# Optimization experiments

Measured on AMD Instinct MI355X. Metric: run time of the kernel, lower is better.

The kernel has to match this reference:

```python
import jax, jax.numpy as jnp
import numpy as np
from jax import lax

# Model dims (match init_kwargs / input_specs)
B, S, D = 4, 2048, 1024
L, H, K = 4, 4, 4
DH = D // H            # 256 head dim
UP = 1344              # ceil(1.3*D/64)*64, gated FFN proj dim
EPS = 1e-5


def _ln(x, w):
    # xlstm LayerNorm: weight only, no bias
    mu = x.mean(-1, keepdims=True)
    var = x.var(-1, keepdims=True)
    return (x - mu) * lax.rsqrt(var + EPS) * w


def _slstm_layer(xn, cw, cb, wi, wf, wz, wo, rk, b, gnw):
    # xn: (B,S,D). Causal depthwise conv1d + swish feeds i/f gates; z/o from xn.
    Bc, Sc, Dc = xn.shape
    xc = lax.conv_general_dilated(
        xn.transpose(0, 2, 1), cw[:, None, :], (1,), [(K - 1, 0)],
        dimension_numbers=("NCH", "OIH", "NCH"), feature_group_count=Dc)
    xc = jax.nn.silu(xc + cb[None, :, None]).transpose(0, 2, 1)
    hx = xc.reshape(Bc, Sc, H, DH)
    hz = xn.reshape(Bc, Sc, H, DH)
    # LinearHeadwiseExpand: block-diagonal per-head linear, no bias
    gi = jnp.einsum("bshd,hod->bsho", hx, wi)
    gf = jnp.einsum("bshd,hod->bsho", hx, wf)
    gz = jnp.einsum("bshd,hod->bsho", hz, wz)
    go = jnp.einsum("bshd,hod->bsho", hz, wo)
    wx = jnp.stack([gi, gf, gz, go], axis=3)  # (B,S,H,4,DH)

    def step(carry, wx_t):
        h, c, n, m = carry  # each (B,H,DH)
        raw = wx_t + jnp.einsum("bhd,hdgo->bhgo", h, rk) + b  # (B,H,4,DH)
        ir, fr, zr, og = raw[:, :, 0], raw[:, :, 1], raw[:, :, 2], raw[:, :, 3]
        lfm = m + jax.nn.log_sigmoid(fr)
        mn = jnp.maximum(ir, lfm)          # stabilizer state
        ig = jnp.exp(ir - mn)
        fg = jnp.exp(lfm - mn)
        cn = fg * c + ig * jnp.tanh(zr)
        nn = fg * n + ig
        hn = jax.nn.sigmoid(og) * cn / nn
        return (hn, cn, nn, mn), hn

    z0 = jnp.zeros((Bc, H, DH), xn.dtype)
    _, ys = lax.scan(step, (z0, z0, z0, z0), jnp.moveaxis(wx, 1, 0))
    y = jnp.moveaxis(ys, 0, 1)  # (B,S,H,DH)
    # MultiHeadLayerNorm / GroupNorm(num_groups=H), weight only
    mu = y.mean(-1, keepdims=True)
    var = y.var(-1, keepdims=True)
    y = (y - mu) * lax.rsqrt(var + EPS) * gnw.reshape(H, DH)
    return y.reshape(Bc, Sc, Dc)


def _ffn(xn, wu, wd):
    u = xn @ wu
    g, v = u[..., :UP], u[..., UP:]
    return (jax.nn.gelu(g, approximate=False) * v) @ wd


def setup_inputs() -> dict:
    key = jax.random.key(0)
    ks = jax.random.split(key, 9)
    sg = DH ** -0.5
    return {
        "x": jax.random.normal(ks[0], (B, S, D), jnp.float32),
        "ln1_w": jnp.ones((L, D), jnp.float32),
        "conv_w": jax.random.normal(ks[1], (L, D, K), jnp.float32) * 0.1,
        "conv_b": jnp.zeros((L, D), jnp.float32),
        "wi": jax.random.normal(ks[2], (L, H, DH, DH), jnp.float32) * sg,
        "wf": jax.random.normal(ks[3], (L, H, DH, DH), jnp.float32) * sg,
        "wz": jax.random.normal(ks[4], (L, H, DH, DH), jnp.float32) * sg,
        "wo": jax.random.normal(ks[5], (L, H, DH, DH), jnp.float32) * sg,
        "rker": jax.random.normal(ks[6], (L, H, DH, 4, DH), jnp.float32) * sg,
        "cell_b": jax.random.normal(ks[7], (L, H, 4, DH), jnp.float32) * 0.1,
        "gn_w": jnp.ones((L, D), jnp.float32),
        "ln2_w": jnp.ones((L, D), jnp.float32),
        "ff_up": jax.random.normal(ks[8], (L, D, 2 * UP), jnp.float32) * (D ** -0.5),
        "ff_down": jax.random.normal(jax.random.fold_in(key, 99), (L, UP, D), jnp.float32) * (UP ** -0.5),
        "post_w": jnp.ones((D,), jnp.float32),
    }


def reference(x, ln1_w, conv_w, conv_b, wi, wf, wz, wo, rker, cell_b, gn_w, ln2_w, ff_up, ff_down, post_w):
    for l in range(L):
        x = x + _slstm_layer(_ln(x, ln1_w[l]), conv_w[l], conv_b[l],
                             wi[l], wf[l], wz[l], wo[l], rker[l], cell_b[l], gn_w[l])
        x = x + _ffn(_ln(x, ln2_w[l]), ff_up[l], ff_down[l])
    return _ln(x, post_w)  # post-blocks norm; dropout is identity in eval
```

## Files before the change

kernel.cpp:

```cpp
#include <hip/hip_runtime.h>
#include <hip/hip_bf16.h>
#include <hip/hip_fp16.h>
#include <math.h>


typedef unsigned int  u32;
typedef unsigned short u16;
typedef __hip_bfloat16 bf16;

typedef short bf16x8 __attribute__((ext_vector_type(8)));
typedef float f32x4  __attribute__((ext_vector_type(4)));
typedef _Float16 half2t __attribute__((ext_vector_type(2)));

#define EPSF 1e-5f
#define SIGF32 0x3F800000u

__device__ __forceinline__ float bfu2f(u16 u){ return __uint_as_float(((u32)u) << 16); }
__device__ __forceinline__ float ldm(const void* p, long i, int f32){
  return f32 ? ((const float*)p)[i] : bfu2f(((const u16*)p)[i]);
}
__device__ __forceinline__ float f16u2f(u16 u){ return (float)__builtin_bit_cast(_Float16, u); }
__device__ __forceinline__ float qdot(u32 w, u32 hp, float acc){
#if defined(__has_builtin)
#if __has_builtin(__builtin_amdgcn_fdot2)
  return __builtin_amdgcn_fdot2(__builtin_bit_cast(half2t, w),
                                __builtin_bit_cast(half2t, hp), acc, false);
#else
  half2t a = __builtin_bit_cast(half2t, w);
  half2t b = __builtin_bit_cast(half2t, hp);
  acc = fmaf((float)a.x, (float)b.x, acc);
  return fmaf((float)a.y, (float)b.y, acc);
#endif
#else
  half2t a = __builtin_bit_cast(half2t, w);
  half2t b = __builtin_bit_cast(half2t, hp);
  acc = fmaf((float)a.x, (float)b.x, acc);
  return fmaf((float)a.y, (float)b.y, acc);
#endif
}

__global__ __launch_bounds__(256) void k_canary(const u32* __restrict__ sig,
                                                void* __restrict__ out, int n, float code){
  int f32 = (sig[0] == SIGF32);
  int i = blockIdx.x*256 + threadIdx.x;
  if (i >= n) return;
  float v = (i == 0) ? code : 0.f;
  if (f32) ((float*)out)[i] = v;
  else     ((bf16*)out)[i]  = __float2bfloat16(v);
}

__global__ __launch_bounds__(256) void k_cast(const void* __restrict__ in,
                                              const u32* __restrict__ sig,
                                              float* __restrict__ out){
  int f32 = (sig[0] == SIGF32);
  long i = (long)blockIdx.x*256 + threadIdx.x;
  if (f32){
    ((float4*)out)[i] = ((const float4*)in)[i];
  } else {
    ushort4 v = ((const ushort4*)in)[i];
    float4 f;
    f.x = bfu2f(v.x); f.y = bfu2f(v.y); f.z = bfu2f(v.z); f.w = bfu2f(v.w);
    ((float4*)out)[i] = f;
  }
}

__global__ __launch_bounds__(256) void k_cvt(const void* __restrict__ src, long off,
                                             const u32* __restrict__ sig,
                                             bf16* __restrict__ dst, int n){
  int f32 = (sig[0] == SIGF32);
  int i = blockIdx.x*256 + threadIdx.x;
  if (i < n) dst[i] = __float2bfloat16(ldm(src, off + i, f32));
}

__global__ __launch_bounds__(256) void k_ln(const float* __restrict__ X,
                                            const void* __restrict__ w, long woff,
                                            const u32* __restrict__ sig,
                                            void* __restrict__ out, int outf){
  int f32 = (sig[0] == SIGF32);
  int row = blockIdx.x, t = threadIdx.x;
  float4 xv = ((const float4*)(X + (long)row*1024))[t];
  float s1 = xv.x + xv.y + xv.z + xv.w;
  float s2 = xv.x*xv.x + xv.y*xv.y + xv.z*xv.z + xv.w*xv.w;
  #pragma unroll
  for (int off = 32; off >= 1; off >>= 1){ s1 += __shfl_xor(s1, off); s2 += __shfl_xor(s2, off); }
  __shared__ float rb[8];
  if ((t & 63) == 0){ rb[t>>6] = s1; rb[4 + (t>>6)] = s2; }
  __syncthreads();
  s1 = rb[0]+rb[1]+rb[2]+rb[3];
  s2 = rb[4]+rb[5]+rb[6]+rb[7];
  float mu  = s1 * (1.f/1024.f);
  float var = s2 * (1.f/1024.f) - mu*mu;
  float rs  = rsqrtf(fmaxf(var, 0.f) + EPSF);
  float xs[4] = {xv.x, xv.y, xv.z, xv.w};
  #pragma unroll
  for (int j = 0; j < 4; j++){
    float val = (xs[j]-mu)*rs*ldm(w, woff + t*4 + j, f32);
    long oi = (long)row*1024 + t*4 + j;
    if (outf && f32) ((float*)out)[oi] = val;
    else             ((bf16*)out)[oi]  = __float2bfloat16(val);
  }
}

__global__ __launch_bounds__(256) void k_conv(const bf16* __restrict__ XN,
                                              const void* __restrict__ cw, long cwoff,
                                              const void* __restrict__ cb, long cboff,
                                              const u32* __restrict__ sig,
                                              bf16* __restrict__ WX){
  int f32 = (sig[0] == SIGF32);
  int idx = blockIdx.x*256 + threadIdx.x;
  int c = idx & 1023;
  int s = (idx >> 10) & 2047;
  int b = idx >> 21;
  float acc = ldm(cb, cboff + c, f32);
  const bf16* xp = XN + idx;
  #pragma unroll
  for (int k = 0; k < 4; k++){
    int sk = s - 3 + k;
    float xv = (sk >= 0) ? (float)xp[(k-3)*1024] : 0.f;
    acc += xv * ldm(cw, cwoff + c*4 + k, f32);
  }
  float sg = 1.f / (1.f + __expf(-acc));
  WX[(long)b*8388608 + (long)(c>>8)*2097152 + (long)s*1024 + 512 + (c & 255)]
      = __float2bfloat16(acc * sg);
}

__global__ __launch_bounds__(256) void k_packrk(const void* __restrict__ rk, long off,
                                                const u32* __restrict__ sig,
                                                u32* __restrict__ rkReg,
                                                u32* __restrict__ rkLds,
                                                u32* __restrict__ rkStr){
  int f32 = (sig[0] == SIGF32);
  int idx = blockIdx.x*256 + threadIdx.x;
  if (idx >= 524288) return;
  int dp = idx & 127;
  int gc = (idx >> 7) & 1023;
  int h  = idx >> 17;
  int g  = gc >> 8, cell = gc & 255;
  int q  = dp >> 5, i = dp & 31;
  int tid = (cell >> 4)*64 + q*16 + (cell & 15);
  long p = off + (long)h*262144 + (long)(dp*2)*1024 + gc;
  float a = ldm(rk, p, f32);
  float b = ldm(rk, p + 1024, f32);
  u32 lo = (u32)__builtin_bit_cast(u16, (_Float16)a);
  u32 hi = (u32)__builtin_bit_cast(u16, (_Float16)b);
  u32 v = lo | (hi << 16);
  if (i < 12){
    rkReg[((long)(g*12 + i)*4 + h)*1024 + tid] = v;
  } else if (i < 16){
    rkLds[(((long)(h*4 + g))*1024 + tid)*4 + (i - 12)] = v;
  } else {
    int c = (i-16) >> 2, j = (i-16) & 3;
    rkStr[(((long)(h*16 + g*4 + c))*1024 + tid)*4 + j] = v;
  }
}

__global__ __launch_bounds__(256) void k_transpose(const void* __restrict__ in, long off,
                                                   const u32* __restrict__ sig,
                                                   bf16* __restrict__ out, int R, int C){
  int f32 = (sig[0] == SIGF32);
  __shared__ bf16 tile[32][33];
  int tx = threadIdx.x & 31, ty = threadIdx.x >> 5;
  int r0 = blockIdx.y*32, c0 = blockIdx.x*32;
  #pragma unroll
  for (int i = 0; i < 4; i++)
    tile[ty + i*8][tx] = __float2bfloat16(ldm(in, off + (long)(r0 + ty + i*8)*C + c0 + tx, f32));
  __syncthreads();
  #pragma unroll
  for (int i = 0; i < 4; i++) out[(long)(c0 + ty + i*8)*R + r0 + tx] = tile[tx][ty + i*8];
}

__global__ __launch_bounds__(256) void k_gemm(const bf16* __restrict__ A, int lda, int aoff, int agate,
                                              const bf16* __restrict__ B0,
                                              const bf16* __restrict__ B1, int ldb, int nsplit,
                                              int K, int mode,
                                              bf16* __restrict__ outb, int ldo, int woff,
                                              float* __restrict__ resid){
  int lane = threadIdx.x & 63, wv = threadIdx.x >> 6;
  int wrow = wv >> 1, wcol = wv & 1;
  int m15 = lane & 15, q = lane >> 4;
  int mBase = blockIdx.x*128 + wrow*64;
  int nBase = blockIdx.y*128 + wcol*64;

  const bf16* Ap[4]; const bf16* Bp[4];
  #pragma unroll
  for (int i = 0; i < 4; i++){
    int row = mBase + i*16 + m15;
    long abase = agate ? ((long)(row >> 11)*8388608 + (long)(row & 2047)*1024)
                       : ((long)row*lda);
    Ap[i] = A + abase + aoff + q*8;
    int n = nBase + i*16 + m15;
    const bf16* bb = (n < nsplit) ? (B0 + (long)n*ldb) : (B1 + (long)(n - nsplit)*ldb);
    Bp[i] = bb + q*8;
  }
  f32x4 acc[4][4];
  f32x4 zero = {0.f, 0.f, 0.f, 0.f};
  #pragma unroll
  for (int i = 0; i < 4; i++)
    #pragma unroll
    for (int j = 0; j < 4; j++) acc[i][j] = zero;

  for (int k0 = 0; k0 < K; k0 += 32){
    bf16x8 af[4], bfg[4];
    #pragma unroll
    for (int i = 0; i < 4; i++){ af[i]  = *reinterpret_cast<const bf16x8*>(Ap[i]); Ap[i] += 32; }
    #pragma unroll
    for (int i = 0; i < 4; i++){ bfg[i] = *reinterpret_cast<const bf16x8*>(Bp[i]); Bp[i] += 32; }
    #pragma unroll
    for (int i = 0; i < 4; i++)
      #pragma unroll
      for (int j = 0; j < 4; j++)
        acc[i][j] = __builtin_amdgcn_mfma_f32_16x16x32_bf16(af[i], bfg[j], acc[i][j], 0, 0, 0);
  }

  #pragma unroll
  for (int i = 0; i < 4; i++){
    #pragma unroll
    for (int j = 0; j < 4; j++){
      #pragma unroll
      for (int r = 0; r < 4; r++){
        int row = mBase + i*16 + q*4 + r;
        int col = nBase + j*16 + m15;
        float v = acc[i][j][r];
        if (mode == 0){
          outb[(long)row*ldo + col] = __float2bfloat16(v);
        } else if (mode == 1){
          outb[(long)(row >> 11)*8388608 + (long)(row & 2047)*1024 + woff + col] = __float2bfloat16(v);
        } else {
          resid[(long)row*1024 + col] += v;
        }
      }
    }
  }
}

__global__ __launch_bounds__(256) void k_act(const bf16* __restrict__ U, bf16* __restrict__ E){
  int idx = blockIdx.x*256 + threadIdx.x;
  int row = idx / 1344;
  int j   = idx - row*1344;
  float g = (float)U[(long)row*2688 + j];
  float v = (float)U[(long)row*2688 + 1344 + j];
  float ge = 0.5f * g * (1.f + erff(g * 0.70710678118654752f));
  E[idx] = __float2bfloat16(ge * v);
}

__global__ __launch_bounds__(1024, 4) void k_recur(bf16* __restrict__ WX,
                                                const u32*  __restrict__ rkReg,
                                                const uint4* __restrict__ rkLdsG,
                                                const uint4* __restrict__ rkStrG,
                                                const void* __restrict__ cb, long cboff,
                                                const u32*  __restrict__ sig,
                                                int szero){
  int f32 = (sig[0] == SIGF32);
  int bh = blockIdx.x;
  int h = bh & 3;
  int tid = threadIdx.x;
  int celllo = tid & 15, q = (tid >> 4) & 3, cellhi = tid >> 6;
  int cell = cellhi*16 + celllo;

  u32 wreg[48];
  {
    const u32* rg = rkReg + h*1024 + tid;
    #pragma unroll
    for (int i = 0; i < 48; i++) wreg[i] = rg[i*4096];
  }
  #pragma unroll
  for (int i = 0; i < 48; i++) asm volatile("" : "+v"(wreg[i]));

  __shared__ __align__(16) uint4 wlds[4096];
  __shared__ __align__(16) u16 hsr[4*264];
  {
    const uint4* srcL = rkLdsG + h*4096;
    #pragma unroll
    for (int g = 0; g < 4; g++) wlds[g*1024 + tid] = srcL[g*1024 + tid];
  }
  if (tid < 528) ((u32*)hsr)[tid] = 0;

  const uint4* st = rkStrG + h*16384 + tid;
  float bias = ldm(cb, cboff + h*1024 + q*256 + cell, f32);

  __syncthreads();

  float c = 0.f, n = 0.f, m = 0.f;
  const u16* wxu = (const u16*)WX + (long)bh*2097152 + q*256 + cell;
  u16* yout = (u16*)WX + (long)bh*2097152 + cell;

  u16 wxc = wxu[0];
  for (int s = 0; s < 2048; s++){
    u16 wxn = wxu[(s < 2047) ? 1024 : 0];
    int off = s * szero;

    const uint4* hq = ((const uint4*)hsr) + q*41;
    uint4 hh0 = hq[0+off], hh1 = hq[1+off], hh2 = hq[2+off], hh3 = hq[3+off];
    uint4 hh4 = hq[4+off], hh5 = hq[5+off], hh6 = hq[6+off], hh7 = hq[7+off];

    float p0, p1, p2, p3;
    #pragma unroll
    for (int g = 0; g < 4; g++){
      uint4 s0 = st[(g*4+0)*1024 + off];
      uint4 s1 = st[(g*4+1)*1024 + off];
      uint4 s2 = st[(g*4+2)*1024 + off];
      uint4 s3 = st[(g*4+3)*1024 + off];
      uint4 wl = wlds[g*1024 + tid + off];
      const u32* wr = wreg + g*12;
      float a = 0.f;
      a = qdot(wr[0],  hh0.x, a); a = qdot(wr[1],  hh0.y, a);
      a = qdot(wr[2],  hh0.z, a); a = qdot(wr[3],  hh0.w, a);
      a = qdot(wr[4],  hh1.x, a); a = qdot(wr[5],  hh1.y, a);
      a = qdot(wr[6],  hh1.z, a); a = qdot(wr[7],  hh1.w, a);
      a = qdot(wr[8],  hh2.x, a); a = qdot(wr[9],  hh2.y, a);
      a = qdot(wr[10], hh2.z, a); a = qdot(wr[11], hh2.w, a);
      a = qdot(wl.x, hh3.x, a); a = qdot(wl.y, hh3.y, a);
      a = qdot(wl.z, hh3.z, a); a = qdot(wl.w, hh3.w, a);
      a = qdot(s0.x, hh4.x, a); a = qdot(s0.y, hh4.y, a);
      a = qdot(s0.z, hh4.z, a); a = qdot(s0.w, hh4.w, a);
      a = qdot(s1.x, hh5.x, a); a = qdot(s1.y, hh5.y, a);
      a = qdot(s1.z, hh5.z, a); a = qdot(s1.w, hh5.w, a);
      a = qdot(s2.x, hh6.x, a); a = qdot(s2.y, hh6.y, a);
      a = qdot(s2.z, hh6.z, a); a = qdot(s2.w, hh6.w, a);
      a = qdot(s3.x, hh7.x, a); a = qdot(s3.y, hh7.y, a);
      a = qdot(s3.z, hh7.z, a); a = qdot(s3.w, hh7.w, a);
      if (g == 0) p0 = a; else if (g == 1) p1 = a; else if (g == 2) p2 = a; else p3 = a;
    }
    float addv = bias + bfu2f(wxc);
    p0 += (q == 0) ? addv : 0.f;
    p1 += (q == 1) ? addv : 0.f;
    p2 += (q == 2) ? addv : 0.f;
    p3 += (q == 3) ? addv : 0.f;
    p0 += __shfl_xor(p0, 16); p0 += __shfl_xor(p0, 32);
    p1 += __shfl_xor(p1, 16); p1 += __shfl_xor(p1, 32);
    p2 += __shfl_xor(p2, 16); p2 += __shfl_xor(p2, 32);
    p3 += __shfl_xor(p3, 16); p3 += __shfl_xor(p3, 32);

    __syncthreads();

    if (q == 0){
      float a0 = p0, a1 = p1, a2 = p2, a3 = p3;
      float e1   = __expf(-fabsf(a1));
      float lsig = fminf(a1, 0.f) - __logf(1.f + e1);
      float lfm  = m + lsig;
      float mn   = fmaxf(a0, lfm);
      float ig   = __expf(a0 - mn);
      float fg   = __expf(lfm - mn);
      float t2   = __expf(-2.f*fabsf(a2));
      float th   = __builtin_copysignf(__fdividef(1.f - t2, 1.f + t2), a2);
      float cn   = fg*c + ig*th;
      float nn   = fg*n + ig;
      float sg   = __fdividef(1.f, 1.f + __expf(-a3));
      float hn   = sg * __fdividef(cn, nn);
      c = cn; n = nn; m = mn;
      u16 h16 = __builtin_bit_cast(u16, (_Float16)hn);
      hsr[0*264 + cell] = h16; hsr[1*264 + cell] = h16;
      hsr[2*264 + cell] = h16; hsr[3*264 + cell] = h16;
      yout[(long)s*1024] = h16;
    }
    __syncthreads();

    wxu += 1024;
    wxc = wxn;
  }
}

__global__ __launch_bounds__(256) void k_gn(const u16* __restrict__ Y,
                                            const void* __restrict__ gnw, long gnoff,
                                            const u32* __restrict__ sig,
                                            float* __restrict__ X){
  int f32 = (sig[0] == SIGF32);
  int r = blockIdx.x;
  int bh = r >> 11, s = r & 2047, b = bh >> 2, h = bh & 3;
  int t = threadIdx.x;
  float y = f16u2f(Y[(long)bh*2097152 + (long)s*1024 + t]);
  float s1 = y, s2 = y*y;
  #pragma unroll
  for (int off = 32; off >= 1; off >>= 1){ s1 += __shfl_xor(s1, off); s2 += __shfl_xor(s2, off); }
  __shared__ float rb[8];
  if ((t & 63) == 0){ rb[t>>6] = s1; rb[4 + (t>>6)] = s2; }
  __syncthreads();
  s1 = rb[0]+rb[1]+rb[2]+rb[3];
  s2 = rb[4]+rb[5]+rb[6]+rb[7];
  float mu  = s1 * (1.f/256.f);
  float var = s2 * (1.f/256.f) - mu*mu;
  float rs  = rsqrtf(fmaxf(var, 0.f) + EPSF);
  float gw  = ldm(gnw, gnoff + h*256 + t, f32);
  X[(long)b*2097152 + (long)s*1024 + h*256 + t] += (y - mu)*rs*gw;
}

extern "C" void kernel_launch(void* const* d_in, const int* in_sizes, int n_in,
                              void* d_out, int out_size, void* d_ws, size_t ws_size,
                              hipStream_t stream){
  const void* x_in   = d_in[0];
  const void* ln1_w  = d_in[1];
  const void* conv_w = d_in[2];
  const void* conv_b = d_in[3];
  const void* wi     = d_in[4];
  const void* wf     = d_in[5];
  const void* wz     = d_in[6];
  const void* wo     = d_in[7];
  const void* rker   = d_in[8];
  const void* cell_b = d_in[9];
  const void* gn_w   = d_in[10];
  const void* ln2_w  = d_in[11];
  const void* ff_up  = d_in[12];
  const void* ff_dn  = d_in[13];
  const void* post_w = d_in[14];
  const u32* sig = (const u32*)ln1_w;

  if (ws_size < 134217728ULL){
    k_canary<<<(out_size+255)/256, 256, 0, stream>>>(sig, d_out, out_size, 4000.f);
    return;
  }
  if (n_in < 15 || in_sizes[0] != 8388608 || in_sizes[8] != 4194304 ||
      in_sizes[12] != 11010048 || out_size != 8388608){
    k_canary<<<(out_size+255)/256, 256, 0, stream>>>(sig, d_out, out_size, 8000.f);
    return;
  }

  char* ws = (char*)d_ws;
  float* X    = (float*)(ws + 0);
  bf16*  XN   = (bf16*) (ws + 33554432);
  u32*   rkReg= (u32*)  (ws + 50331648);
  u32*   rkLds= (u32*)  (ws + 50331648 + 786432);
  u32*   rkStr= (u32*)  (ws + 50331648 + 1048576);
  bf16*  gW   = (bf16*) (ws + 50331648 + 2097152);
  bf16*  fupT = (bf16*) (ws + 50331648 + 4194304);
  bf16*  fdnT = (bf16*) (ws + 50331648 + 9699328);
  bf16*  WX   = (bf16*) (ws + 67108864);
  bf16*  U    = WX;
  bf16*  E    = (bf16*) (ws + 67108864 + 44040192);

  k_cast<<<8192, 256, 0, stream>>>(x_in, sig, X);

  for (int l = 0; l < 4; l++){
    k_ln<<<8192, 256, 0, stream>>>(X, ln1_w, (long)l*1024, sig, XN, 0);
    k_conv<<<32768, 256, 0, stream>>>(XN, conv_w, (long)l*4096, conv_b, (long)l*1024, sig, WX);

    k_cvt<<<1024, 256, 0, stream>>>(wi, (long)l*262144, sig, gW +      0, 262144);
    k_cvt<<<1024, 256, 0, stream>>>(wf, (long)l*262144, sig, gW + 262144, 262144);
    k_cvt<<<1024, 256, 0, stream>>>(wz, (long)l*262144, sig, gW + 524288, 262144);
    k_cvt<<<1024, 256, 0, stream>>>(wo, (long)l*262144, sig, gW + 786432, 262144);

    for (int h = 0; h < 4; h++){
      k_gemm<<<dim3(64,4), 256, 0, stream>>>(WX, 0, h*2097152 + 512, 1,
          gW + h*65536, gW + 262144 + h*65536, 256, 256,
          256, 1, WX, 0, h*2097152 + 0, nullptr);
    }
    k_packrk<<<2048, 256, 0, stream>>>(rker, (long)l*1048576, sig, rkReg, rkLds, rkStr);
    for (int h = 0; h < 4; h++){
      k_gemm<<<dim3(64,4), 256, 0, stream>>>(XN, 1024, h*256, 0,
          gW + 524288 + h*65536, gW + 786432 + h*65536, 256, 256,
          256, 1, WX, 0, h*2097152 + 512, nullptr);
    }

    k_recur<<<16, 1024, 0, stream>>>(WX, rkReg, (const uint4*)rkLds, (const uint4*)rkStr,
                                     cell_b, (long)l*4096, sig, 0);
    k_gn<<<32768, 256, 0, stream>>>((const u16*)WX, gn_w, (long)l*1024, sig, X);

    k_ln<<<8192, 256, 0, stream>>>(X, ln2_w, (long)l*1024, sig, XN, 0);
    k_transpose<<<dim3(84,32), 256, 0, stream>>>(ff_up, (long)l*2752512, sig, fupT, 1024, 2688);
    k_gemm<<<dim3(64,21), 256, 0, stream>>>(XN, 1024, 0, 0, fupT, fupT, 1024, 1<<30,
        1024, 0, U, 2688, 0, nullptr);
    k_act<<<43008, 256, 0, stream>>>(U, E);
    k_transpose<<<dim3(32,42), 256, 0, stream>>>(ff_dn, (long)l*1376256, sig, fdnT, 1344, 1024);
    k_gemm<<<dim3(64,8), 256, 0, stream>>>(E, 1344, 0, 0, fdnT, fdnT, 1344, 1<<30,
        1344, 2, nullptr, 0, 0, X);
  }

  k_ln<<<8192, 256, 0, stream>>>(X, post_w, 0, sig, d_out, 1);
}
```

Baseline: 28.74 ms.

## Use MFMA for sLSTM recurrent matvec, batching all sequences per head

Rewrites the recurrent kernel so each head's block handles all four batch sequences together. The per-step h·R product runs as f16 MFMA 16x16x32 with the recurrent weights held fully in registers, replacing per-thread fdot2 chains fed from registers, LDS and streamed global memory. Results go through LDS so each thread computes the gate update for one (batch, cell), and packrk now writes the MFMA fragment layout. This cuts launched blocks from 16 to 4, so fewer CUs are used, while weight streaming and cross-lane shuffles go away and every thread stays active in the gate stage.

```diff
diff --git a/kernel.cpp b/kernel.cpp
--- a/kernel.cpp
+++ b/kernel.cpp
@@ -9,6 +9,7 @@
 typedef __hip_bfloat16 bf16;
 
 typedef short bf16x8 __attribute__((ext_vector_type(8)));
+typedef _Float16 f16x8 __attribute__((ext_vector_type(8)));
 typedef float f32x4  __attribute__((ext_vector_type(4)));
 typedef _Float16 half2t __attribute__((ext_vector_type(2)));
 
@@ -20,24 +21,6 @@
   return f32 ? ((const float*)p)[i] : bfu2f(((const u16*)p)[i]);
 }
 __device__ __forceinline__ float f16u2f(u16 u){ return (float)__builtin_bit_cast(_Float16, u); }
-__device__ __forceinline__ float qdot(u32 w, u32 hp, float acc){
-#if defined(__has_builtin)
-#if __has_builtin(__builtin_amdgcn_fdot2)
-  return __builtin_amdgcn_fdot2(__builtin_bit_cast(half2t, w),
-                                __builtin_bit_cast(half2t, hp), acc, false);
-#else
-  half2t a = __builtin_bit_cast(half2t, w);
-  half2t b = __builtin_bit_cast(half2t, hp);
-  acc = fmaf((float)a.x, (float)b.x, acc);
-  return fmaf((float)a.y, (float)b.y, acc);
-#endif
-#else
-  half2t a = __builtin_bit_cast(half2t, w);
-  half2t b = __builtin_bit_cast(half2t, hp);
-  acc = fmaf((float)a.x, (float)b.x, acc);
-  return fmaf((float)a.y, (float)b.y, acc);
-#endif
-}
 
 __global__ __launch_bounds__(256) void k_canary(const u32* __restrict__ sig,
                                                 void* __restrict__ out, int n, float code){
@@ -126,32 +109,25 @@
 
 __global__ __launch_bounds__(256) void k_packrk(const void* __restrict__ rk, long off,
                                                 const u32* __restrict__ sig,
-                                                u32* __restrict__ rkReg,
-                                                u32* __restrict__ rkLds,
-                                                u32* __restrict__ rkStr){
+                                                u32* __restrict__ wbuf){
   int f32 = (sig[0] == SIGF32);
   int idx = blockIdx.x*256 + threadIdx.x;
   if (idx >= 524288) return;
-  int dp = idx & 127;
-  int gc = (idx >> 7) & 1023;
-  int h  = idx >> 17;
-  int g  = gc >> 8, cell = gc & 255;
-  int q  = dp >> 5, i = dp & 31;
-  int tid = (cell >> 4)*64 + q*16 + (cell & 15);
-  long p = off + (long)h*262144 + (long)(dp*2)*1024 + gc;
+  int ip   = idx & 3;
+  int lane = (idx >> 2) & 63;
+  int j    = (idx >> 8) & 3;
+  int kt   = (idx >> 10) & 7;
+  int w    = (idx >> 13) & 15;
+  int h    = idx >> 17;
+  int n  = (w*4 + j)*16 + (lane & 15);
+  int k0 = kt*32 + ((lane >> 4) & 3)*8 + ip*2;
+  int g = n >> 8, cell = n & 255;
+  long p = off + (long)h*262144 + (long)k0*1024 + g*256 + cell;
   float a = ldm(rk, p, f32);
   float b = ldm(rk, p + 1024, f32);
   u32 lo = (u32)__builtin_bit_cast(u16, (_Float16)a);
   u32 hi = (u32)__builtin_bit_cast(u16, (_Float16)b);
-  u32 v = lo | (hi << 16);
-  if (i < 12){
-    rkReg[((long)(g*12 + i)*4 + h)*1024 + tid] = v;
-  } else if (i < 16){
-    rkLds[(((long)(h*4 + g))*1024 + tid)*4 + (i - 12)] = v;
-  } else {
-    int c = (i-16) >> 2, j = (i-16) & 3;
-    rkStr[(((long)(h*16 + g*4 + c))*1024 + tid)*4 + j] = v;
-  }
+  wbuf[idx] = lo | (hi << 16);
 }
 
 __global__ __launch_bounds__(256) void k_transpose(const void* __restrict__ in, long off,
@@ -244,119 +220,103 @@
 }
 
 __global__ __launch_bounds__(1024, 4) void k_recur(bf16* __restrict__ WX,
-                                                const u32*  __restrict__ rkReg,
-                                                const uint4* __restrict__ rkLdsG,
-                                                const uint4* __restrict__ rkStrG,
+                                                const uint4* __restrict__ wbufq,
                                                 const void* __restrict__ cb, long cboff,
                                                 const u32*  __restrict__ sig,
                                                 int szero){
   int f32 = (sig[0] == SIGF32);
-  int bh = blockIdx.x;
-  int h = bh & 3;
+  int h = blockIdx.x;
   int tid = threadIdx.x;
-  int celllo = tid & 15, q = (tid >> 4) & 3, cellhi = tid >> 6;
-  int cell = cellhi*16 + celllo;
-
-  u32 wreg[48];
+  int lane = tid & 63, w = tid >> 6;
+  int b = tid >> 8, cell = tid & 255;
+
+  f16x8 wfr[32];
   {
-    const u32* rg = rkReg + h*1024 + tid;
-    #pragma unroll
-    for (int i = 0; i < 48; i++) wreg[i] = rg[i*4096];
-  }
-  #pragma unroll
-  for (int i = 0; i < 48; i++) asm volatile("" : "+v"(wreg[i]));
-
-  __shared__ __align__(16) uint4 wlds[4096];
-  __shared__ __align__(16) u16 hsr[4*264];
-  {
-    const uint4* srcL = rkLdsG + h*4096;
-    #pragma unroll
-    for (int g = 0; g < 4; g++) wlds[g*1024 + tid] = srcL[g*1024 + tid];
-  }
-  if (tid < 528) ((u32*)hsr)[tid] = 0;
-
-  const uint4* st = rkStrG + h*16384 + tid;
-  float bias = ldm(cb, cboff + h*1024 + q*256 + cell, f32);
-
+    const uint4* src = wbufq + (long)(h*16 + w)*32*64 + lane;
+    #pragma unroll
+    for (int f = 0; f < 32; f++){
+      uint4 v = src[f*64];
+      wfr[f] = __builtin_bit_cast(f16x8, v);
+    }
+  }
+  #pragma unroll
+  for (int f = 0; f < 32; f++) asm volatile("" : "+v"(wfr[f]));
+
+  __shared__ __align__(16) u16 hsr[4*272];
+  __shared__ __align__(16) char ylds[1024*40];
+  if (tid < 544) ((u32*)hsr)[tid] = 0u;
+
+  float bs0 = ldm(cb, cboff + h*1024 +   0 + cell, f32);
+  float bs1 = ldm(cb, cboff + h*1024 + 256 + cell, f32);
+  float bs2 = ldm(cb, cboff + h*1024 + 512 + cell, f32);
+  float bs3 = ldm(cb, cboff + h*1024 + 768 + cell, f32);
+
+  const u16* wxu = (const u16*)WX + ((long)b*4 + h)*2097152 + cell;
+  u16* yout = (u16*)WX + ((long)b*4 + h)*2097152 + cell;
+
+  const char* hbase = (const char*)hsr + (lane & 3)*544 + ((lane >> 4) & 3)*16;
+  char* ybase = ylds + ((long)w*64 + lane)*40;
+  const char* yrd = ylds + (long)cell*40 + b*4;
+
+  float c = 0.f, n = 0.f, m = 0.f;
+  u16 wx0 = wxu[0], wx1 = wxu[256], wx2 = wxu[512], wx3 = wxu[768];
   __syncthreads();
 
-  float c = 0.f, n = 0.f, m = 0.f;
-  const u16* wxu = (const u16*)WX + (long)bh*2097152 + q*256 + cell;
-  u16* yout = (u16*)WX + (long)bh*2097152 + cell;
-
-  u16 wxc = wxu[0];
   for (int s = 0; s < 2048; s++){
-    u16 wxn = wxu[(s < 2047) ? 1024 : 0];
+    const u16* wxn = wxu + ((s < 2047) ? 1024 : 0);
+    u16 nx0 = wxn[0], nx1 = wxn[256], nx2 = wxn[512], nx3 = wxn[768];
     int off = s * szero;
 
-    const uint4* hq = ((const uint4*)hsr) + q*41;
-    uint4 hh0 = hq[0+off], hh1 = hq[1+off], hh2 = hq[2+off], hh3 = hq[3+off];
-    uint4 hh4 = hq[4+off], hh5 = hq[5+off], hh6 = hq[6+off], hh7 = hq[7+off];
-
-    float p0, p1, p2, p3;
-    #pragma unroll
-    for (int g = 0; g < 4; g++){
-      uint4 s0 = st[(g*4+0)*1024 + off];
-      uint4 s1 = st[(g*4+1)*1024 + off];
-      uint4 s2 = st[(g*4+2)*1024 + off];
-      uint4 s3 = st[(g*4+3)*1024 + off];
-      uint4 wl = wlds[g*1024 + tid + off];
-      const u32* wr = wreg + g*12;
-      float a = 0.f;
-      a = qdot(wr[0],  hh0.x, a); a = qdot(wr[1],  hh0.y, a);
-      a = qdot(wr[2],  hh0.z, a); a = qdot(wr[3],  hh0.w, a);
-      a = qdot(wr[4],  hh1.x, a); a = qdot(wr[5],  hh1.y, a);
-      a = qdot(wr[6],  hh1.z, a); a = qdot(wr[7],  hh1.w, a);
-      a = qdot(wr[8],  hh2.x, a); a = qdot(wr[9],  hh2.y, a);
-      a = qdot(wr[10], hh2.z, a); a = qdot(wr[11], hh2.w, a);
-      a = qdot(wl.x, hh3.x, a); a = qdot(wl.y, hh3.y, a);
-      a = qdot(wl.z, hh3.z, a); a = qdot(wl.w, hh3.w, a);
-      a = qdot(s0.x, hh4.x, a); a = qdot(s0.y, hh4.y, a);
-      a = qdot(s0.z, hh4.z, a); a = qdot(s0.w, hh4.w, a);
-      a = qdot(s1.x, hh5.x, a); a = qdot(s1.y, hh5.y, a);
-      a = qdot(s1.z, hh5.z, a); a = qdot(s1.w, hh5.w, a);
-      a = qdot(s2.x, hh6.x, a); a = qdot(s2.y, hh6.y, a);
-      a = qdot(s2.z, hh6.z, a); a = qdot(s2.w, hh6.w, a);
-      a = qdot(s3.x, hh7.x, a); a = qdot(s3.y, hh7.y, a);
-      a = qdot(s3.z, hh7.z, a); a = qdot(s3.w, hh7.w, a);
-      if (g == 0) p0 = a; else if (g == 1) p1 = a; else if (g == 2) p2 = a; else p3 = a;
-    }
-    float addv = bias + bfu2f(wxc);
-    p0 += (q == 0) ? addv : 0.f;
-    p1 += (q == 1) ? addv : 0.f;
-    p2 += (q == 2) ? addv : 0.f;
-    p3 += (q == 3) ? addv : 0.f;
-    p0 += __shfl_xor(p0, 16); p0 += __shfl_xor(p0, 32);
-    p1 += __shfl_xor(p1, 16); p1 += __shfl_xor(p1, 32);
-    p2 += __shfl_xor(p2, 16); p2 += __shfl_xor(p2, 32);
-    p3 += __shfl_xor(p3, 16); p3 += __shfl_xor(p3, 32);
-
+    f16x8 af[8];
+    #pragma unroll
+    for (int kt = 0; kt < 8; kt++)
+      af[kt] = *(const f16x8*)(hbase + kt*64 + off);
+
+    f32x4 c0 = {0,0,0,0}, c1 = {0,0,0,0}, c2 = {0,0,0,0}, c3 = {0,0,0,0};
+    #pragma unroll
+    for (int kt = 0; kt < 8; kt++){
+      c0 = __builtin_amdgcn_mfma_f32_16x16x32_f16(af[kt], wfr[kt*4+0], c0, 0, 0, 0);
+      c1 = __builtin_amdgcn_mfma_f32_16x16x32_f16(af[kt], wfr[kt*4+1], c1, 0, 0, 0);
+      c2 = __builtin_amdgcn_mfma_f32_16x16x32_f16(af[kt], wfr[kt*4+2], c2, 0, 0, 0);
+      c3 = __builtin_amdgcn_mfma_f32_16x16x32_f16(af[kt], wfr[kt*4+3], c3, 0, 0, 0);
+    }
+    if (lane < 16){
+      *(float2*)(ybase +    0) = make_float2(c0[0], c0[1]);
+      *(float2*)(ybase +    8) = make_float2(c0[2], c0[3]);
+      *(float2*)(ybase +  640) = make_float2(c1[0], c1[1]);
+      *(float2*)(ybase +  648) = make_float2(c1[2], c1[3]);
+      *(float2*)(ybase + 1280) = make_float2(c2[0], c2[1]);
+      *(float2*)(ybase + 1288) = make_float2(c2[2], c2[3]);
+      *(float2*)(ybase + 1920) = make_float2(c3[0], c3[1]);
+      *(float2*)(ybase + 1928) = make_float2(c3[2], c3[3]);
+    }
     __syncthreads();
 
-    if (q == 0){
-      float a0 = p0, a1 = p1, a2 = p2, a3 = p3;
-      float e1   = __expf(-fabsf(a1));
-      float lsig = fminf(a1, 0.f) - __logf(1.f + e1);
-      float lfm  = m + lsig;
-      float mn   = fmaxf(a0, lfm);
-      float ig   = __expf(a0 - mn);
-      float fg   = __expf(lfm - mn);
-      float t2   = __expf(-2.f*fabsf(a2));
-      float th   = __builtin_copysignf(__fdividef(1.f - t2, 1.f + t2), a2);
-      float cn   = fg*c + ig*th;
-      float nn   = fg*n + ig;
-      float sg   = __fdividef(1.f, 1.f + __expf(-a3));
-      float hn   = sg * __fdividef(cn, nn);
-      c = cn; n = nn; m = mn;
-      u16 h16 = __builtin_bit_cast(u16, (_Float16)hn);
-      hsr[0*264 + cell] = h16; hsr[1*264 + cell] = h16;
-      hsr[2*264 + cell] = h16; hsr[3*264 + cell] = h16;
-      yout[(long)s*1024] = h16;
-    }
+    float a0 = *(const float*)(yrd +     0 + off) + bs0 + bfu2f(wx0);
+    float a1 = *(const float*)(yrd + 10240)       + bs1 + bfu2f(wx1);
+    float a2 = *(const float*)(yrd + 20480)       + bs2 + bfu2f(wx2);
+    float a3 = *(const float*)(yrd + 30720)       + bs3 + bfu2f(wx3);
+
+    float e1   = __expf(-fabsf(a1));
+    float lsig = fminf(a1, 0.f) - __logf(1.f + e1);
+    float lfm  = m + lsig;
+    float mn   = fmaxf(a0, lfm);
+    float ig   = __expf(a0 - mn);
+    float fg   = __expf(lfm - mn);
+    float t2   = __expf(-2.f*fabsf(a2));
+    float th   = __builtin_copysignf(__fdividef(1.f - t2, 1.f + t2), a2);
+    float cn   = fg*c + ig*th;
+    float nn   = fg*n + ig;
+    float sg   = __fdividef(1.f, 1.f + __expf(-a3));
+    float hn   = sg * __fdividef(cn, nn);
+    c = cn; n = nn; m = mn;
+    u16 h16 = __builtin_bit_cast(u16, (_Float16)hn);
+    hsr[b*272 + cell] = h16;
+    yout[(long)s*1024] = h16;
     __syncthreads();
 
     wxu += 1024;
-    wxc = wxn;
+    wx0 = nx0; wx1 = nx1; wx2 = nx2; wx3 = nx3;
   }
 }
 
@@ -417,9 +377,7 @@
   char* ws = (char*)d_ws;
   float* X    = (float*)(ws + 0);
   bf16*  XN   = (bf16*) (ws + 33554432);
-  u32*   rkReg= (u32*)  (ws + 50331648);
-  u32*   rkLds= (u32*)  (ws + 50331648 + 786432);
-  u32*   rkStr= (u32*)  (ws + 50331648 + 1048576);
+  u32*   wbuf = (u32*)  (ws + 50331648);
   bf16*  gW   = (bf16*) (ws + 50331648 + 2097152);
   bf16*  fupT = (bf16*) (ws + 50331648 + 4194304);
   bf16*  fdnT = (bf16*) (ws + 50331648 + 9699328);
@@ -443,15 +401,15 @@
           gW + h*65536, gW + 262144 + h*65536, 256, 256,
           256, 1, WX, 0, h*2097152 + 0, nullptr);
     }
-    k_packrk<<<2048, 256, 0, stream>>>(rker, (long)l*1048576, sig, rkReg, rkLds, rkStr);
+    k_packrk<<<2048, 256, 0, stream>>>(rker, (long)l*1048576, sig, wbuf);
     for (int h = 0; h < 4; h++){
       k_gemm<<<dim3(64,4), 256, 0, stream>>>(XN, 1024, h*256, 0,
           gW + 524288 + h*65536, gW + 786432 + h*65536, 256, 256,
           256, 1, WX, 0, h*2097152 + 512, nullptr);
     }
 
-    k_recur<<<16, 1024, 0, stream>>>(WX, rkReg, (const uint4*)rkLds, (const uint4*)rkStr,
-                                     cell_b, (long)l*4096, sig, 0);
+    k_recur<<<4, 1024, 0, stream>>>(WX, (const uint4*)wbuf,
+                                    cell_b, (long)l*4096, sig, 0);
     k_gn<<<32768, 256, 0, stream>>>((const u16*)WX, gn_w, (long)l*1024, sig, X);
 
     k_ln<<<8192, 256, 0, stream>>>(X, ln2_w, (long)l*1024, sig, XN, 0);
```

After: 55.54 ms. +93.3%, slower.
